# Kernel optimization log

Measured on AMD Instinct MI355X. Metric: run time of the kernel, lower is better.

Reference implementation:

```python
import jax, jax.numpy as jnp
import numpy as np

N_NODES = 100000
N_EDGES = 1600000
D = 64
BN_EPS = 1e-5


def setup_inputs() -> dict:
    key = jax.random.key(0)
    ks = jax.random.split(key, 10)
    s = 1.0 / np.sqrt(D)
    return {
        "features": jax.random.normal(ks[0], (N_NODES, D), dtype=jnp.float32),
        "src": jax.random.randint(ks[1], (N_EDGES,), 0, N_NODES, dtype=jnp.int32),
        "dst": jax.random.randint(ks[2], (N_EDGES,), 0, N_NODES, dtype=jnp.int32),
        "eps": jnp.zeros((), dtype=jnp.float32),
        "W1": jax.random.uniform(ks[3], (D, D), jnp.float32, -s, s),
        "b1": jax.random.uniform(ks[4], (D,), jnp.float32, -s, s),
        "W2": jax.random.uniform(ks[5], (D, D), jnp.float32, -s, s),
        "b2": jax.random.uniform(ks[6], (D,), jnp.float32, -s, s),
        "gamma": jnp.ones((D,), dtype=jnp.float32),
        "beta": jnp.zeros((D,), dtype=jnp.float32),
    }


def reference(features, src, dst, eps, W1, b1, W2, b2, gamma, beta):
    h_in = features
    # message passing: gather src node features, scatter-sum to dst (fn.copy_u + fn.sum)
    neigh = jax.ops.segment_sum(features[src], dst, num_segments=N_NODES)  # [N, D]
    # eps-weighted self term
    h = (1.0 + eps) * features + neigh
    # apply_func MLP: Linear -> ReLU -> Linear
    h = jnp.maximum(h @ W1 + b1, 0.0) @ W2 + b2
    # BatchNorm1d over nodes (training-mode batch statistics)
    mean = jnp.mean(h, axis=0)
    var = jnp.var(h, axis=0)
    h = (h - mean) * jax.lax.rsqrt(var + BN_EPS) * gamma + beta
    # activation
    h = jnp.maximum(h, 0.0)
    # residual (indim == outdim)
    h = h_in + h
    # dropout p=0 -> identity
    return h
```

## Files before the change

kernel.cpp:

```cpp
#include <hip/hip_runtime.h>
#include <hip/hip_fp16.h>

#define N_NODES 100000
#define N_EDGES 1600000
#define D 64
#define BN_EPS 1e-5f
#define NSHARD 8

#define NBKT 256
#define NPB 391
#define BKT_CAP 8192
#define NBBLK 391
#define SORT_T 1024

typedef _Float16 half8 __attribute__((ext_vector_type(8)));
typedef float f32x4 __attribute__((ext_vector_type(4)));

__global__ __launch_bounds__(256) void prep_k(
    const int* __restrict__ src, const int* __restrict__ dst,
    int* __restrict__ bkt_cnt, int* __restrict__ bktbuf,
    const float* __restrict__ feat, __half* __restrict__ feat16,
    const float* __restrict__ W1, const float* __restrict__ W2,
    _Float16* __restrict__ w1t, _Float16* __restrict__ w2t)
{
    __shared__ int h[NBKT], base[NBKT], cur[NBKT];
    const int blk = blockIdx.x;
    const int t = threadIdx.x;

    if (blk < NBBLK) {
        h[t] = 0; cur[t] = 0;
        __syncthreads();
        const int e0 = blk * 4096;
        int pk[16], b[16];
        #pragma unroll
        for (int i = 0; i < 16; ++i) {
            int e = e0 + i * 256 + t;
            if (e < N_EDGES) {
                int d = dst[e];
                b[i] = d / NPB;
                pk[i] = (src[e] << 9) | (d - b[i] * NPB);
                atomicAdd(&h[b[i]], 1);
            } else {
                b[i] = -1;
            }
        }
        __syncthreads();
        base[t] = atomicAdd(&bkt_cnt[t], h[t]);
        __syncthreads();
        #pragma unroll
        for (int i = 0; i < 16; ++i) {
            if (b[i] >= 0) {
                int p = atomicAdd(&cur[b[i]], 1);
                bktbuf[(size_t)b[i] * BKT_CAP + base[b[i]] + p] = pk[i];
            }
        }
    } else if (blk < NBBLK + 3125) {
        size_t i = ((size_t)(blk - NBBLK) * 256 + t) * 8;
        if (i < (size_t)N_NODES * D) {
            float4 v0 = *(const float4*)(feat + i);
            float4 v1 = *(const float4*)(feat + i + 4);
            __half2 o[4];
            o[0] = __floats2half2_rn(v0.x, v0.y);
            o[1] = __floats2half2_rn(v0.z, v0.w);
            o[2] = __floats2half2_rn(v1.x, v1.y);
            o[3] = __floats2half2_rn(v1.z, v1.w);
            *(float4*)(feat16 + i) = *(float4*)o;
        }
    } else {
        const int n = t >> 2;
        const int k0 = (t & 3) * 16;
        _Float16 o1[16], o2[16];
        #pragma unroll
        for (int j = 0; j < 16; ++j) {
            o1[j] = (_Float16)W1[(k0 + j) * 64 + n];
            o2[j] = (_Float16)W2[(k0 + j) * 64 + n];
        }
        #pragma unroll
        for (int j = 0; j < 16; j += 8) {
            *(half8*)(w1t + n * 64 + k0 + j) = *(half8*)&o1[j];
            *(half8*)(w2t + n * 64 + k0 + j) = *(half8*)&o2[j];
        }
    }
}

__device__ __forceinline__ int wscan_incl(int x, int lane)
{
    #pragma unroll
    for (int off = 1; off < 64; off <<= 1) {
        int v = __shfl_up(x, off, 64);
        if (lane >= off) x += v;
    }
    return x;
}

__global__ __launch_bounds__(SORT_T) void sortp_k(
    const int* __restrict__ bktbuf, const int* __restrict__ bkt_cnt,
    int* __restrict__ rowptr, int* __restrict__ col, float* __restrict__ stats)
{
    __shared__ int h[NPB];
    __shared__ int cur[NPB];
    __shared__ int wsum[16];

    const int b    = blockIdx.x;
    const int t    = threadIdx.x;
    const int lane = t & 63;
    const int wv   = t >> 6;
    const int nb0  = b * NPB;
    const int nodes_in = min(NPB, N_NODES - nb0);
    const int cnt = min(bkt_cnt[b], BKT_CAP);
    const int* buf = bktbuf + (size_t)b * BKT_CAP;

    if (b == 0) stats[t] = 0.f;

    int ci = 0;
    if (t < NBKT && t < b) ci = min(bkt_cnt[t], BKT_CAP);
    #pragma unroll
    for (int off = 32; off >= 1; off >>= 1) ci += __shfl_xor(ci, off, 64);
    if (lane == 0) wsum[wv] = ci;
    if (t < NPB) h[t] = 0;
    __syncthreads();
    const int gbase = wsum[0] + wsum[1] + wsum[2] + wsum[3];

    for (int i = t; i < cnt; i += SORT_T)
        atomicAdd(&h[buf[i] & 511], 1);
    __syncthreads();

    int a = 0, x = 0;
    if (wv < 7) {
        a = (t < NPB) ? h[t] : 0;
        x = wscan_incl(a, lane);
        if (lane == 63) wsum[wv] = x;
    }
    __syncthreads();
    if (wv < 7) {
        int offs = 0;
        for (int i = 0; i < wv; ++i) offs += wsum[i];
        const int excl = x - a + offs;
        if (t < NPB) {
            cur[t] = excl;
            if (t < nodes_in) rowptr[nb0 + t] = gbase + excl;
        }
    }
    if (b == NBKT - 1 && t == 0) rowptr[N_NODES] = N_EDGES;
    __syncthreads();

    for (int i = t; i < cnt; i += SORT_T) {
        int pk = buf[i];
        int slot = atomicAdd(&cur[pk & 511], 1);
        col[gbase + slot] = pk >> 9;
    }
}

__device__ __forceinline__ void acc16(float* a, float4 r0, float4 r1)
{
    const __half2* h0 = (const __half2*)&r0;
    const __half2* h1 = (const __half2*)&r1;
    #pragma unroll
    for (int i = 0; i < 4; ++i) {
        float2 f = __half22float2(h0[i]);
        a[2 * i]     += f.x;
        a[2 * i + 1] += f.y;
    }
    #pragma unroll
    for (int i = 0; i < 4; ++i) {
        float2 f = __half22float2(h1[i]);
        a[8 + 2 * i]     += f.x;
        a[8 + 2 * i + 1] += f.y;
    }
}

__global__ __launch_bounds__(64, 4) void gmlp_k(
    const __half* __restrict__ feat16, const int* __restrict__ rowptr,
    const int* __restrict__ col, const float* __restrict__ epsp,
    const _Float16* __restrict__ w1t, const _Float16* __restrict__ w2t,
    const float* __restrict__ b1, const float* __restrict__ b2,
    __half* __restrict__ h216, float* __restrict__ stats)
{
    __shared__ __align__(16) _Float16 xts[16 * 72];

    const int t  = threadIdx.x;
    const int nb = blockIdx.x * 16;

    {
        const int nl   = t >> 2;
        const int node = nb + nl;
        const int c    = (t & 3) << 4;
        const int lo = rowptr[node];
        const int hi = rowptr[node + 1];
        float a[16];
        #pragma unroll
        for (int i = 0; i < 16; ++i) a[i] = 0.f;

        int e = lo;
        for (; e + 3 < hi; e += 4) {
            const int s0 = col[e], s1 = col[e + 1], s2 = col[e + 2], s3 = col[e + 3];
            const __half* p0 = feat16 + (size_t)s0 * 64 + c;
            const __half* p1 = feat16 + (size_t)s1 * 64 + c;
            const __half* p2 = feat16 + (size_t)s2 * 64 + c;
            const __half* p3 = feat16 + (size_t)s3 * 64 + c;
            float4 r00 = *(const float4*)(p0), r01 = *(const float4*)(p0 + 8);
            float4 r10 = *(const float4*)(p1), r11 = *(const float4*)(p1 + 8);
            float4 r20 = *(const float4*)(p2), r21 = *(const float4*)(p2 + 8);
            float4 r30 = *(const float4*)(p3), r31 = *(const float4*)(p3 + 8);
            acc16(a, r00, r01);
            acc16(a, r10, r11);
            acc16(a, r20, r21);
            acc16(a, r30, r31);
        }
        for (; e < hi; ++e) {
            const __half* p = feat16 + (size_t)col[e] * 64 + c;
            float4 r0 = *(const float4*)(p), r1 = *(const float4*)(p + 8);
            acc16(a, r0, r1);
        }

        const float epsv = 1.0f + epsp[0];
        const size_t gb = (size_t)node * 64 + c;
        float4 s0 = *(const float4*)(feat16 + gb);
        float4 s1 = *(const float4*)(feat16 + gb + 8);
        const __half2* h0 = (const __half2*)&s0;
        const __half2* h1 = (const __half2*)&s1;
        __half2 o[8];
        #pragma unroll
        for (int i = 0; i < 4; ++i) {
            float2 f = __half22float2(h0[i]);
            o[i] = __floats2half2_rn(fmaf(epsv, f.x, a[2 * i]),
                                     fmaf(epsv, f.y, a[2 * i + 1]));
        }
        #pragma unroll
        for (int i = 0; i < 4; ++i) {
            float2 f = __half22float2(h1[i]);
            o[4 + i] = __floats2half2_rn(fmaf(epsv, f.x, a[8 + 2 * i]),
                                         fmaf(epsv, f.y, a[8 + 2 * i + 1]));
        }
        *(float4*)&xts[nl * 72 + c]     = *(float4*)&o[0];
        *(float4*)&xts[nl * 72 + c + 8] = *(float4*)&o[4];
    }
    asm volatile("s_waitcnt lgkmcnt(0)" ::: "memory");
    __builtin_amdgcn_sched_barrier(0);

    const int m = t & 15;
    const int q = t >> 4;

    const _Float16* xa = &xts[m * 72 + q * 8];
    half8 a0 = *(const half8*)(xa);
    half8 a1 = *(const half8*)(xa + 32);

    f32x4 acc[4];
    #pragma unroll
    for (int jt = 0; jt < 4; ++jt) {
        const float bias = b1[jt * 16 + m];
        acc[jt] = (f32x4){bias, bias, bias, bias};
        const _Float16* bw = w1t + (jt * 16 + m) * 64 + q * 8;
        half8 bf0 = *(const half8*)(bw);
        half8 bf1 = *(const half8*)(bw + 32);
        acc[jt] = __builtin_amdgcn_mfma_f32_16x16x32_f16(a0, bf0, acc[jt], 0, 0, 0);
        acc[jt] = __builtin_amdgcn_mfma_f32_16x16x32_f16(a1, bf1, acc[jt], 0, 0, 0);
    }

    #pragma unroll
    for (int jt = 0; jt < 4; ++jt)
        #pragma unroll
        for (int r = 0; r < 4; ++r)
            xts[(q * 4 + r) * 72 + jt * 16 + m] =
                (_Float16)fmaxf(acc[jt][r], 0.0f);
    asm volatile("s_waitcnt lgkmcnt(0)" ::: "memory");
    __builtin_amdgcn_sched_barrier(0);

    const _Float16* xw = &xts[m * 72 + q * 8];
    half8 c0 = *(const half8*)(xw);
    half8 c1 = *(const half8*)(xw + 32);

    f32x4 acc2[4];
    #pragma unroll
    for (int jt = 0; jt < 4; ++jt) {
        const float bias = b2[jt * 16 + m];
        acc2[jt] = (f32x4){bias, bias, bias, bias};
        const _Float16* bw = w2t + (jt * 16 + m) * 64 + q * 8;
        half8 bf0 = *(const half8*)(bw);
        half8 bf1 = *(const half8*)(bw + 32);
        acc2[jt] = __builtin_amdgcn_mfma_f32_16x16x32_f16(c0, bf0, acc2[jt], 0, 0, 0);
        acc2[jt] = __builtin_amdgcn_mfma_f32_16x16x32_f16(c1, bf1, acc2[jt], 0, 0, 0);
    }
    asm volatile("s_waitcnt lgkmcnt(0)" ::: "memory");
    __builtin_amdgcn_sched_barrier(0);

    float psums[4], psqs[4];
    #pragma unroll
    for (int jt = 0; jt < 4; ++jt) {
        float ps = 0.f, pq = 0.f;
        #pragma unroll
        for (int r = 0; r < 4; ++r) {
            const int row = q * 4 + r;
            const float v = acc2[jt][r];
            ps += v;
            pq += v * v;
            xts[row * 72 + jt * 16 + m] = (_Float16)v;
        }
        ps += __shfl_xor(ps, 16, 64); ps += __shfl_xor(ps, 32, 64);
        pq += __shfl_xor(pq, 16, 64); pq += __shfl_xor(pq, 32, 64);
        psums[jt] = ps; psqs[jt] = pq;
    }
    if (t < 16) {
        float* sp = stats + (size_t)(blockIdx.x & (NSHARD - 1)) * 128;
        #pragma unroll
        for (int jt = 0; jt < 4; ++jt) {
            unsafeAtomicAdd(sp + jt * 16 + t,      psums[jt]);
            unsafeAtomicAdd(sp + 64 + jt * 16 + t, psqs[jt]);
        }
    }
    asm volatile("s_waitcnt lgkmcnt(0)" ::: "memory");
    __builtin_amdgcn_sched_barrier(0);

    {
        const int rr = t >> 2;
        const int cc = (t & 3) * 16;
        const int gn = nb + rr;
        float4 r0 = *(const float4*)&xts[rr * 72 + cc];
        float4 r1 = *(const float4*)&xts[rr * 72 + cc + 8];
        *(float4*)(h216 + (size_t)gn * 64 + cc)     = r0;
        *(float4*)(h216 + (size_t)gn * 64 + cc + 8) = r1;
    }
}

__global__ __launch_bounds__(256) void finish16_k(
    const float* __restrict__ feat, const __half* __restrict__ h216,
    const float* __restrict__ stats, const float* __restrict__ gamma,
    const float* __restrict__ beta, float* __restrict__ out)
{
    __shared__ float scs[64], shs[64];
    const int t = threadIdx.x;
    if (t < 64) {
        float s = 0.f, q = 0.f;
        #pragma unroll
        for (int c = 0; c < NSHARD; ++c) {
            s += stats[c * 128 + t];
            q += stats[c * 128 + 64 + t];
        }
        const float invN = 1.0f / (float)N_NODES;
        const float mean = s * invN;
        const float var  = q * invN - mean * mean;
        const float scale = gamma[t] * rsqrtf(var + BN_EPS);
        scs[t] = scale;
        shs[t] = beta[t] - mean * scale;
    }
    __syncthreads();
    size_t i = (size_t)blockIdx.x * 256 + t;
    if (i < (size_t)N_NODES * D / 4) {
        int j = (int)((i * 4) & 63);
        const __half2* hp = (const __half2*)(h216 + i * 4);
        float2 h0 = __half22float2(hp[0]);
        float2 h1 = __half22float2(hp[1]);
        float4 f = *(const float4*)(feat + i * 4);
        float4 o;
        o.x = fmaxf(fmaf(h0.x, scs[j + 0], shs[j + 0]), 0.f) + f.x;
        o.y = fmaxf(fmaf(h0.y, scs[j + 1], shs[j + 1]), 0.f) + f.y;
        o.z = fmaxf(fmaf(h1.x, scs[j + 2], shs[j + 2]), 0.f) + f.z;
        o.w = fmaxf(fmaf(h1.y, scs[j + 3], shs[j + 3]), 0.f) + f.w;
        *(float4*)(out + i * 4) = o;
    }
}

#define OCAP 7680

__global__ void bnstats_k(const float* __restrict__ stats,
                          const float* __restrict__ gamma,
                          const float* __restrict__ beta,
                          float* __restrict__ sf)
{
    int j = threadIdx.x;
    float s = 0.f, q = 0.f;
    for (int c = 0; c < NSHARD; ++c) {
        s += stats[c * 128 + j];
        q += stats[c * 128 + 64 + j];
    }
    const float invN = 1.0f / (float)N_NODES;
    float mean  = s * invN;
    float var   = q * invN - mean * mean;
    float scale = gamma[j] * rsqrtf(var + BN_EPS);
    sf[j]      = scale;
    sf[64 + j] = beta[j] - mean * scale;
}

__global__ __launch_bounds__(256) void bucket2_k(
    const int* __restrict__ src, const int* __restrict__ dst,
    int* __restrict__ bkt_cnt, int2* __restrict__ bktbuf)
{
    __shared__ int h[NBKT], base[NBKT], cur[NBKT];
    const int t = threadIdx.x;
    h[t] = 0; cur[t] = 0;
    __syncthreads();
    const int e0 = blockIdx.x * 4096;
    int s[16], d[16], b[16];
    #pragma unroll
    for (int i = 0; i < 16; ++i) {
        int e = e0 + i * 256 + t;
        if (e < N_EDGES) {
            s[i] = src[e];
            d[i] = dst[e];
            b[i] = d[i] / NPB;
            atomicAdd(&h[b[i]], 1);
        } else {
            b[i] = -1;
        }
    }
    __syncthreads();
    base[t] = atomicAdd(&bkt_cnt[t], h[t]);
    __syncthreads();
    #pragma unroll
    for (int i = 0; i < 16; ++i) {
        if (b[i] >= 0) {
            int p = atomicAdd(&cur[b[i]], 1);
            bktbuf[(size_t)b[i] * OCAP + base[b[i]] + p] = make_int2(s[i], d[i]);
        }
    }
}

__global__ __launch_bounds__(SORT_T) void sort2_k(
    const int2* __restrict__ bktbuf, const int* __restrict__ bkt_cnt,
    int* __restrict__ rowptr, int* __restrict__ col)
{
    __shared__ int h[NPB];
    __shared__ int cur[NPB];
    __shared__ int part[SORT_T];
    __shared__ int bsc[NBKT];

    const int b = blockIdx.x;
    const int t = threadIdx.x;
    const int nb0 = b * NPB;
    const int nodes_in = min(NPB, N_NODES - nb0);
    const int cnt = bkt_cnt[b];
    const int2* buf = bktbuf + (size_t)b * OCAP;

    if (t < NBKT) bsc[t] = bkt_cnt[t];
    __syncthreads();
    for (int off = 1; off < NBKT; off <<= 1) {
        int x = 0;
        if (t < NBKT) {
            x = bsc[t];
            if (t >= off) x += bsc[t - off];
        }
        __syncthreads();
        if (t < NBKT) bsc[t] = x;
        __syncthreads();
    }
    const int gbase = bsc[b] - cnt;

    if (t < NPB) h[t] = 0;
    __syncthreads();

    for (int i = t; i < cnt; i += SORT_T)
        atomicAdd(&h[buf[i].y - nb0], 1);
    __syncthreads();

    int a = (t < NPB) ? h[t] : 0;
    part[t] = a;
    __syncthreads();
    for (int off = 1; off < SORT_T; off <<= 1) {
        int x = part[t];
        int u = (t >= off) ? part[t - off] : 0;
        __syncthreads();
        part[t] = x + u;
        __syncthreads();
    }
    int excl = part[t] - a;
    if (t < NPB) {
        cur[t] = excl;
        if (t < nodes_in) rowptr[nb0 + t] = gbase + excl;
    }
    if (b == NBKT - 1 && t == 0) rowptr[N_NODES] = N_EDGES;
    __syncthreads();

    for (int i = t; i < cnt; i += SORT_T) {
        int2 r = buf[i];
        int slot = atomicAdd(&cur[r.y - nb0], 1);
        col[gbase + slot] = r.x;
    }
}

__global__ __launch_bounds__(256) void gather32_k(
    const float* __restrict__ feat, const int* __restrict__ rowptr,
    const int* __restrict__ col, const float* __restrict__ epsp,
    float* __restrict__ x)
{
    int node = blockIdx.x * 4 + (threadIdx.x >> 6);
    int lane = threadIdx.x & 63;
    if (node >= N_NODES) return;
    int g = lane >> 4;
    int c = (lane & 15) << 2;
    int lo = rowptr[node];
    int hi = rowptr[node + 1];
    float ax = 0.f, ay = 0.f, az = 0.f, aw = 0.f;
    int e = lo + g;
    for (; e + 4 < hi; e += 8) {
        int s0 = col[e];
        int s1 = col[e + 4];
        float4 v0 = *(const float4*)(feat + (size_t)s0 * D + c);
        float4 v1 = *(const float4*)(feat + (size_t)s1 * D + c);
        ax += v0.x; ay += v0.y; az += v0.z; aw += v0.w;
        ax += v1.x; ay += v1.y; az += v1.z; aw += v1.w;
    }
    if (e < hi) {
        float4 v = *(const float4*)(feat + (size_t)col[e] * D + c);
        ax += v.x; ay += v.y; az += v.z; aw += v.w;
    }
    #pragma unroll
    for (int off = 16; off <= 32; off <<= 1) {
        ax += __shfl_xor(ax, off, 64);
        ay += __shfl_xor(ay, off, 64);
        az += __shfl_xor(az, off, 64);
        aw += __shfl_xor(aw, off, 64);
    }
    if (g == 0) {
        float4 f = *(const float4*)(feat + (size_t)node * D + c);
        const float epsv = 1.0f + epsp[0];
        float4 r;
        r.x = fmaf(epsv, f.x, ax);
        r.y = fmaf(epsv, f.y, ay);
        r.z = fmaf(epsv, f.z, az);
        r.w = fmaf(epsv, f.w, aw);
        *(float4*)(x + (size_t)node * D + c) = r;
    }
}

__global__ __launch_bounds__(256) void mlp32_k(
    const float* __restrict__ x,
    const float* __restrict__ W1, const float* __restrict__ b1,
    const float* __restrict__ W2, const float* __restrict__ b2,
    float* __restrict__ h2out, float* __restrict__ stats)
{
    __shared__ float W1s[64 * 68];
    __shared__ float W2s[64 * 68];
    __shared__ float xs[64 * 65];
    __shared__ float b1s[64], b2s[64];

    const int t  = threadIdx.x;
    const int nb = blockIdx.x * 64;

    #pragma unroll
    for (int i = 0; i < 4; ++i) {
        int l  = t + i * 256;
        int k  = l >> 4;
        int j4 = (l & 15) << 2;
        *(float4*)(&W1s[k * 68 + j4]) = *(const float4*)(W1 + k * 64 + j4);
        *(float4*)(&W2s[k * 68 + j4]) = *(const float4*)(W2 + k * 64 + j4);
    }
    if (t < 64)       b1s[t]      = b1[t];
    else if (t < 128) b2s[t - 64] = b2[t - 64];

    #pragma unroll
    for (int i = 0; i < 2; ++i) {
        int n  = (t >> 3) + i * 32;
        int k8 = (t & 7) << 3;
        int gn = nb + n;
        float4 a = make_float4(0.f, 0.f, 0.f, 0.f), b = a;
        if (gn < N_NODES) {
            a = *(const float4*)(x + (size_t)gn * D + k8);
            b = *(const float4*)(x + (size_t)gn * D + k8 + 4);
        }
        *(float4*)&xs[n * 65 + k8]     = a;
        *(float4*)&xs[n * 65 + k8 + 4] = b;
    }
    __syncthreads();

    const int n0 = (t & 15) << 2;
    const int j0 = (t >> 4) << 2;
    const float* xr0 = &xs[(n0 + 0) * 65];
    const float* xr1 = &xs[(n0 + 1) * 65];
    const float* xr2 = &xs[(n0 + 2) * 65];
    const float* xr3 = &xs[(n0 + 3) * 65];

    float acc[4][4];
    #pragma unroll
    for (int a = 0; a < 4; ++a)
        #pragma unroll
        for (int b = 0; b < 4; ++b)
            acc[a][b] = b1s[j0 + b];

    #pragma unroll 8
    for (int k = 0; k < 64; ++k) {
        const float4 w = *(const float4*)(&W1s[k * 68 + j0]);
        const float x0 = xr0[k], x1 = xr1[k], x2 = xr2[k], x3 = xr3[k];
        acc[0][0] = fmaf(x0, w.x, acc[0][0]); acc[0][1] = fmaf(x0, w.y, acc[0][1]);
        acc[0][2] = fmaf(x0, w.z, acc[0][2]); acc[0][3] = fmaf(x0, w.w, acc[0][3]);
        acc[1][0] = fmaf(x1, w.x, acc[1][0]); acc[1][1] = fmaf(x1, w.y, acc[1][1]);
        acc[1][2] = fmaf(x1, w.z, acc[1][2]); acc[1][3] = fmaf(x1, w.w, acc[1][3]);
        acc[2][0] = fmaf(x2, w.x, acc[2][0]); acc[2][1] = fmaf(x2, w.y, acc[2][1]);
        acc[2][2] = fmaf(x2, w.z, acc[2][2]); acc[2][3] = fmaf(x2, w.w, acc[2][3]);
        acc[3][0] = fmaf(x3, w.x, acc[3][0]); acc[3][1] = fmaf(x3, w.y, acc[3][1]);
        acc[3][2] = fmaf(x3, w.z, acc[3][2]); acc[3][3] = fmaf(x3, w.w, acc[3][3]);
    }

    __syncthreads();
    #pragma unroll
    for (int a = 0; a < 4; ++a)
        #pragma unroll
        for (int b = 0; b < 4; ++b)
            xs[(n0 + a) * 65 + j0 + b] = fmaxf(acc[a][b], 0.0f);
    __syncthreads();

    float acc2[4][4];
    #pragma unroll
    for (int a = 0; a < 4; ++a)
        #pragma unroll
        for (int b = 0; b < 4; ++b)
            acc2[a][b] = b2s[j0 + b];

    #pragma unroll 8
    for (int k = 0; k < 64; ++k) {
        const float4 w = *(const float4*)(&W2s[k * 68 + j0]);
        const float x0 = xr0[k], x1 = xr1[k], x2 = xr2[k], x3 = xr3[k];
        acc2[0][0] = fmaf(x0, w.x, acc2[0][0]); acc2[0][1] = fmaf(x0, w.y, acc2[0][1]);
        acc2[0][2] = fmaf(x0, w.z, acc2[0][2]); acc2[0][3] = fmaf(x0, w.w, acc2[0][3]);
        acc2[1][0] = fmaf(x1, w.x, acc2[1][0]); acc2[1][1] = fmaf(x1, w.y, acc2[1][1]);
        acc2[1][2] = fmaf(x1, w.z, acc2[1][2]); acc2[1][3] = fmaf(x1, w.w, acc2[1][3]);
        acc2[2][0] = fmaf(x2, w.x, acc2[2][0]); acc2[2][1] = fmaf(x2, w.y, acc2[2][1]);
        acc2[2][2] = fmaf(x2, w.z, acc2[2][2]); acc2[2][3] = fmaf(x2, w.w, acc2[2][3]);
        acc2[3][0] = fmaf(x3, w.x, acc2[3][0]); acc2[3][1] = fmaf(x3, w.y, acc2[3][1]);
        acc2[3][2] = fmaf(x3, w.z, acc2[3][2]); acc2[3][3] = fmaf(x3, w.w, acc2[3][3]);
    }

    float psum[4] = {0.f, 0.f, 0.f, 0.f};
    float psq[4]  = {0.f, 0.f, 0.f, 0.f};
    #pragma unroll
    for (int a = 0; a < 4; ++a) {
        int gn = nb + n0 + a;
        if (gn < N_NODES) {
            float4 hh;
            hh.x = acc2[a][0]; hh.y = acc2[a][1]; hh.z = acc2[a][2]; hh.w = acc2[a][3];
            *(float4*)(h2out + (size_t)gn * 64 + j0) = hh;
            psum[0] += hh.x; psq[0] += hh.x * hh.x;
            psum[1] += hh.y; psq[1] += hh.y * hh.y;
            psum[2] += hh.z; psq[2] += hh.z * hh.z;
            psum[3] += hh.w; psq[3] += hh.w * hh.w;
        }
    }
    #pragma unroll
    for (int off = 8; off >= 1; off >>= 1)
        #pragma unroll
        for (int b = 0; b < 4; ++b) {
            psum[b] += __shfl_down(psum[b], off, 16);
            psq[b]  += __shfl_down(psq[b],  off, 16);
        }
    if ((t & 15) == 0) {
        float* sp = stats + (size_t)(blockIdx.x & (NSHARD - 1)) * 128;
        #pragma unroll
        for (int b = 0; b < 4; ++b) {
            unsafeAtomicAdd(sp + j0 + b,      psum[b]);
            unsafeAtomicAdd(sp + 64 + j0 + b, psq[b]);
        }
    }
}

__global__ __launch_bounds__(256) void finish_k(
    const float* __restrict__ feat, const float* __restrict__ sf,
    float* __restrict__ out)
{
    __shared__ float scs[64], shs[64];
    if (threadIdx.x < 64) {
        scs[threadIdx.x] = sf[threadIdx.x];
        shs[threadIdx.x] = sf[64 + threadIdx.x];
    }
    __syncthreads();
    size_t i = (size_t)blockIdx.x * 256 + threadIdx.x;
    if (i < (size_t)N_NODES * D / 4) {
        int j = (int)((i * 4) & 63);
        float4 h = *(float4*)(out + i * 4);
        float4 f = *(const float4*)(feat + i * 4);
        h.x = fmaxf(fmaf(h.x, scs[j + 0], shs[j + 0]), 0.f) + f.x;
        h.y = fmaxf(fmaf(h.y, scs[j + 1], shs[j + 1]), 0.f) + f.y;
        h.z = fmaxf(fmaf(h.z, scs[j + 2], shs[j + 2]), 0.f) + f.z;
        h.w = fmaxf(fmaf(h.w, scs[j + 3], shs[j + 3]), 0.f) + f.w;
        *(float4*)(out + i * 4) = h;
    }
}

extern "C" void kernel_launch(void* const* d_in, const int* in_sizes, int n_in,
                              void* d_out, int out_size, void* d_ws, size_t ws_size,
                              hipStream_t stream)
{
    const float* feat  = (const float*)d_in[0];
    const int*   src   = (const int*)d_in[1];
    const int*   dst   = (const int*)d_in[2];
    const float* eps   = (const float*)d_in[3];
    const float* W1    = (const float*)d_in[4];
    const float* b1    = (const float*)d_in[5];
    const float* W2    = (const float*)d_in[6];
    const float* b2    = (const float*)d_in[7];
    const float* gamma = (const float*)d_in[8];
    const float* beta  = (const float*)d_in[9];
    float* out = (float*)d_out;

    const size_t BKTSZ  = (size_t)NBKT * BKT_CAP * sizeof(int);
    const size_t F16SZ  = (size_t)N_NODES * D * sizeof(__half);
    const size_t COLSZ  = (size_t)N_EDGES * sizeof(int);
    const size_t RPSZ   = ((size_t)(N_NODES + 1) * sizeof(int) + 15) & ~(size_t)15;
    const size_t STATSZ = (size_t)NSHARD * 128 * sizeof(float);
    const size_t CNTSZ  = (size_t)NBKT * sizeof(int);
    const size_t TAIL   = STATSZ + CNTSZ + 128 * 4 + 2 * 4096 * sizeof(_Float16) + 256;
    const size_t need   = BKTSZ + 2 * F16SZ + COLSZ + RPSZ + TAIL;

    if (ws_size >= need) {
        char* p = (char*)d_ws;
        int*    bktbuf  = (int*)p;
        __half* h216    = (__half*)p;
        __half* feat16  = (__half*)(p + BKTSZ + F16SZ);
        int*    col     = (int*)(p + BKTSZ + 2 * F16SZ);
        int*    rowptr  = (int*)(p + BKTSZ + 2 * F16SZ + COLSZ);
        float*  stats   = (float*)(p + BKTSZ + 2 * F16SZ + COLSZ + RPSZ);
        int*    bkt_cnt = (int*)(stats + NSHARD * 128);
        float*  sf      = (float*)(bkt_cnt + NBKT);
        _Float16* w1t   = (_Float16*)(sf + 128);
        _Float16* w2t   = w1t + 4096;
        (void)sf;

        hipMemsetAsync(bkt_cnt, 0, CNTSZ, stream);
        prep_k<<<NBBLK + 3125 + 1, 256, 0, stream>>>(src, dst, bkt_cnt, bktbuf,
                                                     feat, feat16, W1, W2, w1t, w2t);
        sortp_k<<<NBKT, SORT_T, 0, stream>>>(bktbuf, bkt_cnt, rowptr, col, stats);
        gmlp_k<<<N_NODES / 16, 64, 0, stream>>>(feat16, rowptr, col, eps,
                                                w1t, w2t, b1, b2, h216, stats);
        finish16_k<<<(N_NODES * D / 4 + 255) / 256, 256, 0, stream>>>(
            feat, h216, stats, gamma, beta, out);
    } else {
        const size_t X32SZ = (size_t)N_NODES * D * sizeof(float);
        char* p = (char*)d_ws;
        float* x32    = (float*)p;
        int2*  bktbuf = (int2*)p;
        int*   col    = (int*)(p + X32SZ);
        int*   rowptr = col + N_EDGES;
        float* stats  = (float*)(rowptr + N_NODES + 1);
        int*   bkt_cnt = (int*)(stats + NSHARD * 128);
        float* sf     = (float*)(bkt_cnt + NBKT);

        hipMemsetAsync(stats, 0, STATSZ + NBKT * 4, stream);
        bucket2_k<<<(N_EDGES + 4095) / 4096, 256, 0, stream>>>(src, dst, bkt_cnt, bktbuf);
        sort2_k<<<NBKT, SORT_T, 0, stream>>>(bktbuf, bkt_cnt, rowptr, col);
        gather32_k<<<(N_NODES + 3) / 4, 256, 0, stream>>>(feat, rowptr, col, eps, x32);
        mlp32_k<<<(N_NODES + 63) / 64, 256, 0, stream>>>(x32, W1, b1, W2, b2, out, stats);
        bnstats_k<<<1, 64, 0, stream>>>(stats, gamma, beta, sf);
        finish_k<<<(N_NODES * D / 4 + 255) / 256, 256, 0, stream>>>(feat, sf, out);
    }
}
```

Before: 201.8 us.

## Split fused gather-MLP kernel into separate gather and MFMA MLP kernels

Replaces the single 64-thread-per-block kernel, which did the neighbour gather and then the two-layer MFMA MLP, with two kernels: a 256-thread gather kernel that writes the aggregated fp16 input to a workspace buffer, and a 256-thread MLP kernel where each wavefront handles 16 rows. The aim is better occupancy and latency hiding for the irregular gather, which the small fused blocks limited. The cost is an extra fp16 activation write and read through global memory plus one more launch. The workspace is re-laid out so the new buffer aliases the enlarged bucket buffer and the MLP output aliases the fp16 features.

```diff
diff --git a/kernel.cpp b/kernel.cpp
--- a/kernel.cpp
+++ b/kernel.cpp
@@ -9,7 +9,7 @@
 
 #define NBKT 256
 #define NPB 391
-#define BKT_CAP 8192
+#define BKT_CAP 13056
 #define NBBLK 391
 #define SORT_T 1024
 
@@ -169,81 +169,87 @@
     }
 }
 
-__global__ __launch_bounds__(64, 4) void gmlp_k(
+__global__ __launch_bounds__(256) void gatherq_k(
     const __half* __restrict__ feat16, const int* __restrict__ rowptr,
     const int* __restrict__ col, const float* __restrict__ epsp,
+    __half* __restrict__ x16)
+{
+    const int t = threadIdx.x;
+    const int node = blockIdx.x * 64 + (t >> 2);
+    if (node >= N_NODES) return;
+    const int c = (t & 3) << 4;
+
+    const int lo = rowptr[node];
+    const int hi = rowptr[node + 1];
+
+    float a[16];
+    #pragma unroll
+    for (int i = 0; i < 16; ++i) a[i] = 0.f;
+
+    int e = lo;
+    for (; e + 3 < hi; e += 4) {
+        const int s0 = col[e], s1 = col[e + 1], s2 = col[e + 2], s3 = col[e + 3];
+        const __half* p0 = feat16 + (size_t)s0 * 64 + c;
+        const __half* p1 = feat16 + (size_t)s1 * 64 + c;
+        const __half* p2 = feat16 + (size_t)s2 * 64 + c;
+        const __half* p3 = feat16 + (size_t)s3 * 64 + c;
+        float4 r00 = *(const float4*)(p0), r01 = *(const float4*)(p0 + 8);
+        float4 r10 = *(const float4*)(p1), r11 = *(const float4*)(p1 + 8);
+        float4 r20 = *(const float4*)(p2), r21 = *(const float4*)(p2 + 8);
+        float4 r30 = *(const float4*)(p3), r31 = *(const float4*)(p3 + 8);
+        acc16(a, r00, r01);
+        acc16(a, r10, r11);
+        acc16(a, r20, r21);
+        acc16(a, r30, r31);
+    }
+    for (; e < hi; ++e) {
+        const __half* p = feat16 + (size_t)col[e] * 64 + c;
+        float4 r0 = *(const float4*)(p), r1 = *(const float4*)(p + 8);
+        acc16(a, r0, r1);
+    }
+
+    const float epsv = 1.0f + epsp[0];
+    const size_t gb = (size_t)node * 64 + c;
+    float4 s0 = *(const float4*)(feat16 + gb);
+    float4 s1 = *(const float4*)(feat16 + gb + 8);
+    const __half2* h0 = (const __half2*)&s0;
+    const __half2* h1 = (const __half2*)&s1;
+    __half2 o[8];
+    #pragma unroll
+    for (int i = 0; i < 4; ++i) {
+        float2 f = __half22float2(h0[i]);
+        o[i] = __floats2half2_rn(fmaf(epsv, f.x, a[2 * i]),
+                                 fmaf(epsv, f.y, a[2 * i + 1]));
+    }
+    #pragma unroll
+    for (int i = 0; i < 4; ++i) {
+        float2 f = __half22float2(h1[i]);
+        o[4 + i] = __floats2half2_rn(fmaf(epsv, f.x, a[8 + 2 * i]),
+                                     fmaf(epsv, f.y, a[8 + 2 * i + 1]));
+    }
+    *(float4*)(x16 + gb)     = *(float4*)&o[0];
+    *(float4*)(x16 + gb + 8) = *(float4*)&o[4];
+}
+
+__global__ __launch_bounds__(256) void mfma_mlp2_k(
+    const __half* __restrict__ x16,
     const _Float16* __restrict__ w1t, const _Float16* __restrict__ w2t,
     const float* __restrict__ b1, const float* __restrict__ b2,
     __half* __restrict__ h216, float* __restrict__ stats)
 {
-    __shared__ __align__(16) _Float16 xts[16 * 72];
-
-    const int t  = threadIdx.x;
-    const int nb = blockIdx.x * 16;
-
-    {
-        const int nl   = t >> 2;
-        const int node = nb + nl;
-        const int c    = (t & 3) << 4;
-        const int lo = rowptr[node];
-        const int hi = rowptr[node + 1];
-        float a[16];
-        #pragma unroll
-        for (int i = 0; i < 16; ++i) a[i] = 0.f;
-
-        int e = lo;
-        for (; e + 3 < hi; e += 4) {
-            const int s0 = col[e], s1 = col[e + 1], s2 = col[e + 2], s3 = col[e + 3];
-            const __half* p0 = feat16 + (size_t)s0 * 64 + c;
-            const __half* p1 = feat16 + (size_t)s1 * 64 + c;
-            const __half* p2 = feat16 + (size_t)s2 * 64 + c;
-            const __half* p3 = feat16 + (size_t)s3 * 64 + c;
-            float4 r00 = *(const float4*)(p0), r01 = *(const float4*)(p0 + 8);
-            float4 r10 = *(const float4*)(p1), r11 = *(const float4*)(p1 + 8);
-            float4 r20 = *(const float4*)(p2), r21 = *(const float4*)(p2 + 8);
-            float4 r30 = *(const float4*)(p3), r31 = *(const float4*)(p3 + 8);
-            acc16(a, r00, r01);
-            acc16(a, r10, r11);
-            acc16(a, r20, r21);
-            acc16(a, r30, r31);
-        }
-        for (; e < hi; ++e) {
-            const __half* p = feat16 + (size_t)col[e] * 64 + c;
-            float4 r0 = *(const float4*)(p), r1 = *(const float4*)(p + 8);
-            acc16(a, r0, r1);
-        }
-
-        const float epsv = 1.0f + epsp[0];
-        const size_t gb = (size_t)node * 64 + c;
-        float4 s0 = *(const float4*)(feat16 + gb);
-        float4 s1 = *(const float4*)(feat16 + gb + 8);
-        const __half2* h0 = (const __half2*)&s0;
-        const __half2* h1 = (const __half2*)&s1;
-        __half2 o[8];
-        #pragma unroll
-        for (int i = 0; i < 4; ++i) {
-            float2 f = __half22float2(h0[i]);
-            o[i] = __floats2half2_rn(fmaf(epsv, f.x, a[2 * i]),
-                                     fmaf(epsv, f.y, a[2 * i + 1]));
-        }
-        #pragma unroll
-        for (int i = 0; i < 4; ++i) {
-            float2 f = __half22float2(h1[i]);
-            o[4 + i] = __floats2half2_rn(fmaf(epsv, f.x, a[8 + 2 * i]),
-                                         fmaf(epsv, f.y, a[8 + 2 * i + 1]));
-        }
-        *(float4*)&xts[nl * 72 + c]     = *(float4*)&o[0];
-        *(float4*)&xts[nl * 72 + c + 8] = *(float4*)&o[4];
-    }
-    asm volatile("s_waitcnt lgkmcnt(0)" ::: "memory");
-    __builtin_amdgcn_sched_barrier(0);
-
-    const int m = t & 15;
-    const int q = t >> 4;
-
-    const _Float16* xa = &xts[m * 72 + q * 8];
-    half8 a0 = *(const half8*)(xa);
-    half8 a1 = *(const half8*)(xa + 32);
+    __shared__ __align__(16) _Float16 xts[64 * 72];
+
+    const int t    = threadIdx.x;
+    const int w    = t >> 6;
+    const int lane = t & 63;
+    const int m    = lane & 15;
+    const int q    = lane >> 4;
+    const int rbase = w * 16;
+    const int nb   = blockIdx.x * 64;
+
+    const _Float16* xg = (const _Float16*)x16 + (size_t)(nb + rbase + m) * 64 + q * 8;
+    half8 a0 = *(const half8*)(xg);
+    half8 a1 = *(const half8*)(xg + 32);
 
     f32x4 acc[4];
     #pragma unroll
@@ -261,12 +267,12 @@
     for (int jt = 0; jt < 4; ++jt)
         #pragma unroll
         for (int r = 0; r < 4; ++r)
-            xts[(q * 4 + r) * 72 + jt * 16 + m] =
+            xts[(rbase + q * 4 + r) * 72 + jt * 16 + m] =
                 (_Float16)fmaxf(acc[jt][r], 0.0f);
     asm volatile("s_waitcnt lgkmcnt(0)" ::: "memory");
     __builtin_amdgcn_sched_barrier(0);
 
-    const _Float16* xw = &xts[m * 72 + q * 8];
+    const _Float16* xw = &xts[(rbase + m) * 72 + q * 8];
     half8 c0 = *(const half8*)(xw);
     half8 c1 = *(const half8*)(xw + 32);
 
@@ -290,35 +296,38 @@
         float ps = 0.f, pq = 0.f;
         #pragma unroll
         for (int r = 0; r < 4; ++r) {
-            const int row = q * 4 + r;
+            const int row = rbase + q * 4 + r;
             const float v = acc2[jt][r];
-            ps += v;
-            pq += v * v;
+            const float vv = (nb + row < N_NODES) ? v : 0.f;
+            ps += vv;
+            pq += vv * vv;
             xts[row * 72 + jt * 16 + m] = (_Float16)v;
         }
         ps += __shfl_xor(ps, 16, 64); ps += __shfl_xor(ps, 32, 64);
         pq += __shfl_xor(pq, 16, 64); pq += __shfl_xor(pq, 32, 64);
         psums[jt] = ps; psqs[jt] = pq;
     }
-    if (t < 16) {
+    if (lane < 16) {
         float* sp = stats + (size_t)(blockIdx.x & (NSHARD - 1)) * 128;
         #pragma unroll
         for (int jt = 0; jt < 4; ++jt) {
-            unsafeAtomicAdd(sp + jt * 16 + t,      psums[jt]);
-            unsafeAtomicAdd(sp + 64 + jt * 16 + t, psqs[jt]);
+            unsafeAtomicAdd(sp + jt * 16 + lane,      psums[jt]);
+            unsafeAtomicAdd(sp + 64 + jt * 16 + lane, psqs[jt]);
         }
     }
     asm volatile("s_waitcnt lgkmcnt(0)" ::: "memory");
     __builtin_amdgcn_sched_barrier(0);
 
     {
-        const int rr = t >> 2;
-        const int cc = (t & 3) * 16;
-        const int gn = nb + rr;
-        float4 r0 = *(const float4*)&xts[rr * 72 + cc];
-        float4 r1 = *(const float4*)&xts[rr * 72 + cc + 8];
-        *(float4*)(h216 + (size_t)gn * 64 + cc)     = r0;
-        *(float4*)(h216 + (size_t)gn * 64 + cc + 8) = r1;
+        const int rr = lane >> 2;
+        const int cc = (lane & 3) * 16;
+        const int gn = nb + rbase + rr;
+        if (gn < N_NODES) {
+            float4 r0 = *(const float4*)&xts[(rbase + rr) * 72 + cc];
+            float4 r1 = *(const float4*)&xts[(rbase + rr) * 72 + cc + 8];
+            *(float4*)(h216 + (size_t)gn * 64 + cc)     = r0;
+            *(float4*)(h216 + (size_t)gn * 64 + cc + 8) = r1;
+        }
     }
 }
 
@@ -697,16 +706,17 @@
     const size_t STATSZ = (size_t)NSHARD * 128 * sizeof(float);
     const size_t CNTSZ  = (size_t)NBKT * sizeof(int);
     const size_t TAIL   = STATSZ + CNTSZ + 128 * 4 + 2 * 4096 * sizeof(_Float16) + 256;
-    const size_t need   = BKTSZ + 2 * F16SZ + COLSZ + RPSZ + TAIL;
+    const size_t need   = BKTSZ + F16SZ + COLSZ + RPSZ + TAIL;
 
     if (ws_size >= need) {
         char* p = (char*)d_ws;
         int*    bktbuf  = (int*)p;
-        __half* h216    = (__half*)p;
-        __half* feat16  = (__half*)(p + BKTSZ + F16SZ);
-        int*    col     = (int*)(p + BKTSZ + 2 * F16SZ);
-        int*    rowptr  = (int*)(p + BKTSZ + 2 * F16SZ + COLSZ);
-        float*  stats   = (float*)(p + BKTSZ + 2 * F16SZ + COLSZ + RPSZ);
+        __half* x16     = (__half*)p;
+        __half* feat16  = (__half*)(p + BKTSZ);
+        __half* h216    = feat16;
+        int*    col     = (int*)(p + BKTSZ + F16SZ);
+        int*    rowptr  = (int*)(p + BKTSZ + F16SZ + COLSZ);
+        float*  stats   = (float*)(p + BKTSZ + F16SZ + COLSZ + RPSZ);
         int*    bkt_cnt = (int*)(stats + NSHARD * 128);
         float*  sf      = (float*)(bkt_cnt + NBKT);
         _Float16* w1t   = (_Float16*)(sf + 128);
@@ -717,8 +727,8 @@
         prep_k<<<NBBLK + 3125 + 1, 256, 0, stream>>>(src, dst, bkt_cnt, bktbuf,
                                                      feat, feat16, W1, W2, w1t, w2t);
         sortp_k<<<NBKT, SORT_T, 0, stream>>>(bktbuf, bkt_cnt, rowptr, col, stats);
-        gmlp_k<<<N_NODES / 16, 64, 0, stream>>>(feat16, rowptr, col, eps,
-                                                w1t, w2t, b1, b2, h216, stats);
+        gatherq_k<<<(N_NODES + 63) / 64, 256, 0, stream>>>(feat16, rowptr, col, eps, x16);
+        mfma_mlp2_k<<<(N_NODES + 63) / 64, 256, 0, stream>>>(x16, w1t, w2t, b1, b2, h216, stats);
         finish16_k<<<(N_NODES * D / 4 + 255) / 256, 256, 0, stream>>>(
             feat, h216, stats, gamma, beta, out);
     } else {
```

Result: slower. 222.1 us (+10.0%).
